# Kernel tuning notes

Measured on AMD Instinct MI355X. Metric: run time of the kernel, lower is better.

The kernel has to match this reference:

```python
import jax, jax.numpy as jnp
import numpy as np

NUM_HEADS = 16


def setup_inputs() -> dict:
    key = jax.random.key(0)
    ks = jax.random.split(key, 4)
    B, S, D = 2, 2048, 1024
    scale = 1.0 / np.sqrt(D)
    x = jax.random.normal(ks[0], (B, S, D), dtype=jnp.float32)
    Wq = jax.random.normal(ks[1], (D, D), dtype=jnp.float32) * scale
    Wk = jax.random.normal(ks[2], (D, D), dtype=jnp.float32) * scale
    Wv = jax.random.normal(ks[3], (D, D), dtype=jnp.float32) * scale
    bq = jnp.zeros((D,), dtype=jnp.float32)
    bk = jnp.zeros((D,), dtype=jnp.float32)
    bv = jnp.zeros((D,), dtype=jnp.float32)
    return {"x": x, "Wq": Wq, "bq": bq, "Wk": Wk, "bk": bk, "Wv": Wv, "bv": bv}


def _split_heads(t, H):
    B, S, D = t.shape
    return t.reshape(B, S, H, D // H).transpose(0, 2, 1, 3)  # (B,H,S,depth)


def reference(x, Wq, bq, Wk, bk, Wv, bv):
    H = NUM_HEADS
    B, S, D = x.shape
    depth = D // H
    q = _split_heads(x @ Wq + bq, H)
    k = _split_heads(x @ Wk + bk, H)
    v = _split_heads(x @ Wv + bv, H)
    # causal mask: strictly-upper-triangular ones, added as finfo.min * mask
    mask = 1.0 - jnp.tril(jnp.ones((S, S), dtype=jnp.float32))
    scores = jnp.einsum("bhqd,bhkd->bhqk", q, k) / jnp.sqrt(jnp.float32(depth))
    scores = scores + jnp.float32(np.finfo(np.float32).min) * mask
    probs = jax.nn.softmax(scores, axis=-1)
    att = jnp.einsum("bhqk,bhkd->bhqd", probs, v)
    return att.transpose(0, 2, 1, 3).reshape(B, S, D)
```

## Files before the change

### kernel.cpp

```cpp
#include <hip/hip_runtime.h>
#include <hip/hip_bf16.h>

#define B_ 2
#define S_ 2048
#define D_ 1024
#define H_ 16
#define DH 64
#define M_ (B_*S_)
#define NT_ (S_/64)

using bf16x8 = __attribute__((ext_vector_type(8))) __bf16;
using bf16x4 = __attribute__((ext_vector_type(4))) __bf16;
using f32x4  = __attribute__((ext_vector_type(4))) float;

__device__ __forceinline__ int swz(int row) { return ((row ^ (row >> 3)) & 7) << 3; }

__device__ __forceinline__ void glds16(const __bf16* g, __bf16* l) {
#if __has_builtin(__builtin_amdgcn_global_load_lds)
  __builtin_amdgcn_global_load_lds(
      (const __attribute__((address_space(1))) unsigned int*)g,
      (__attribute__((address_space(3))) unsigned int*)l, 16, 0, 0);
#else
  *(bf16x8*)l = *(const bf16x8*)g;
#endif
}

#define NBX 2048
__global__ __launch_bounds__(256) void prep(
    const float* __restrict__ x, const float* __restrict__ Wq,
    const float* __restrict__ Wk, const float* __restrict__ Wv,
    __bf16* __restrict__ xb, __bf16* __restrict__ wt) {
  int bid = blockIdx.x, tid = threadIdx.x;
  if (bid < NBX) {
    int idx = bid * 256 + tid;
    int m = idx >> 7, k = (idx & 127) * 8;
    float4 a = *(const float4*)&x[(size_t)m * D_ + k];
    float4 b = *(const float4*)&x[(size_t)m * D_ + k + 4];
    bf16x8 o;
    o[0]=(__bf16)a.x; o[1]=(__bf16)a.y; o[2]=(__bf16)a.z; o[3]=(__bf16)a.w;
    o[4]=(__bf16)b.x; o[5]=(__bf16)b.y; o[6]=(__bf16)b.z; o[7]=(__bf16)b.w;
    *(bf16x8*)&xb[(size_t)m * D_ + (k & ~63) + ((k & 63) ^ swz(m))] = o;
    return;
  }
  int wb = bid - NBX;
  int z = wb >> 8;
  int kt = (wb & 255) >> 4, nt = wb & 15;
  const float* __restrict__ W = (z == 0) ? Wq : (z == 1) ? Wk : Wv;
  __bf16* __restrict__ Wt = wt + (size_t)z * D_ * D_;
  __shared__ __bf16 Lt[64 * 66];
  int k0 = kt * 64, n0 = nt * 64;
  #pragma unroll
  for (int i = 0; i < 4; ++i) {
    int f4 = i * 256 + tid;
    int r = f4 >> 4, c4 = (f4 & 15) * 4;
    float4 v = *(const float4*)&W[(size_t)(k0 + r) * D_ + n0 + c4];
    Lt[(c4 + 0) * 66 + r] = (__bf16)v.x;
    Lt[(c4 + 1) * 66 + r] = (__bf16)v.y;
    Lt[(c4 + 2) * 66 + r] = (__bf16)v.z;
    Lt[(c4 + 3) * 66 + r] = (__bf16)v.w;
  }
  __syncthreads();
  #pragma unroll
  for (int i = 0; i < 2; ++i) {
    int idx = i * 256 + tid;
    int n = idx >> 3, kc = (idx & 7) * 8;
    int nf = n0 + n;
    bf16x8 o;
    #pragma unroll
    for (int j = 0; j < 8; ++j) o[j] = Lt[n * 66 + kc + j];
    *(bf16x8*)&Wt[(size_t)nf * D_ + k0 + (kc ^ swz(nf))] = o;
  }
}

#define BM 256
#define BN 256
#define BK 64
#define NKT (D_/BK)
#define NWG 192

__global__ __launch_bounds__(512) void qkv_gemm(
    const __bf16* __restrict__ xb, const __bf16* __restrict__ wt,
    const float* __restrict__ bq, const float* __restrict__ bk,
    const float* __restrict__ bv, __bf16* __restrict__ qk,
    __bf16* __restrict__ vt) {
  int flat = blockIdx.x;
  int sid = (flat & 7) * (NWG / 8) + (flat >> 3);
  int z = sid >> 6;
  int rem = sid & 63;
  int my = rem >> 2, nx = rem & 3;

  const __bf16* __restrict__ Wt = wt + (size_t)z * D_ * D_;
  const float* __restrict__ bias = (z == 0) ? bq : (z == 1) ? bk : bv;
  const float scale = (z == 0) ? 0.18033688f : 1.0f;

  __shared__ __bf16 SB[4][BM * BK];

  int tid = threadIdx.x, lane = tid & 63, w = tid >> 6;
  const int g = lane >> 4, ql = lane & 15;
  int m0 = my * BM, n0 = nx * BN;
  int wr = (w >> 2) * 128;
  int wc = (w & 3) * 64;

  f32x4 acc[8][4] = {};
  bf16x8 bfr[4];

#define STAGE2(buf, kt, p)                                                    \
  {                                                                           \
    int k0 = (kt) * BK;                                                       \
    _Pragma("unroll")                                                         \
    for (int q = 0; q < 2; ++q) {                                             \
      int c = 2 * (p) + q;                                                    \
      int e = ((c & 3) * 512 + tid) * 8;                                      \
      int row = e >> 6, col = e & 63;                                         \
      if (c < 4) glds16(&xb[(size_t)(m0 + row) * D_ + k0 + col], &SB[buf][e]);\
      else glds16(&Wt[(size_t)(n0 + row) * D_ + k0 + col], &SB[2 + (buf)][e]);\
    }                                                                         \
  }

#define DSB(buf, kk)                                                          \
  {                                                                           \
    _Pragma("unroll")                                                         \
    for (int ni = 0; ni < 4; ++ni) {                                          \
      int col = wc + ni * 16 + ql;                                            \
      bfr[ni] = *(const bf16x8*)&SB[2 + (buf)][col * 64 +                     \
                (((kk) * 32 + g * 8) ^ swz(col))];                            \
    }                                                                         \
  }

#define DSA4(buf, kk, mh, af)                                                 \
  {                                                                           \
    _Pragma("unroll")                                                         \
    for (int mi = 0; mi < 4; ++mi) {                                          \
      int row = wr + ((mh) * 4 + mi) * 16 + ql;                               \
      af[mi] = *(const bf16x8*)&SB[buf][row * 64 +                            \
               (((kk) * 32 + g * 8) ^ swz(row))];                             \
    }                                                                         \
  }

#define MFMA16(af, mh)                                                        \
  {                                                                           \
    __builtin_amdgcn_s_setprio(1);                                            \
    _Pragma("unroll")                                                         \
    for (int mi = 0; mi < 4; ++mi)                                            \
      _Pragma("unroll")                                                       \
      for (int ni = 0; ni < 4; ++ni)                                          \
        acc[(mh) * 4 + mi][ni] = __builtin_amdgcn_mfma_f32_16x16x32_bf16(     \
            af[mi], bfr[ni], acc[(mh) * 4 + mi][ni], 0, 0, 0);                \
    __builtin_amdgcn_s_setprio(0);                                            \
  }

  #pragma unroll
  for (int p = 0; p < 4; ++p) STAGE2(0, 0, p);

  for (int t = 0; t < NKT; ++t) {
    int cb = t & 1, nb = cb ^ 1;
    bool pf = (t + 1 < NKT);
    bf16x8 af[4];
    if (pf) STAGE2(nb, t + 1, 0);
    __builtin_amdgcn_sched_barrier(0);
    if (pf) { asm volatile("s_waitcnt vmcnt(2)" ::: "memory"); }
    else    { asm volatile("s_waitcnt vmcnt(0)" ::: "memory"); }
    __builtin_amdgcn_sched_barrier(0);
    __builtin_amdgcn_s_barrier();
    __builtin_amdgcn_sched_barrier(0);
    DSB(cb, 0);
    DSA4(cb, 0, 0, af);
    MFMA16(af, 0);
    if (pf) STAGE2(nb, t + 1, 1);
    DSA4(cb, 0, 1, af);
    __builtin_amdgcn_s_barrier();
    MFMA16(af, 1);
    if (pf) STAGE2(nb, t + 1, 2);
    DSB(cb, 1);
    DSA4(cb, 1, 0, af);
    __builtin_amdgcn_s_barrier();
    MFMA16(af, 0);
    if (pf) STAGE2(nb, t + 1, 3);
    DSA4(cb, 1, 1, af);
    __builtin_amdgcn_s_barrier();
    MFMA16(af, 1);
  }
  __syncthreads();
#undef STAGE2
#undef DSB
#undef DSA4
#undef MFMA16

  __bf16* Lt = &SB[0][0];
  const int b = m0 >> 11;
  const int sbase = m0 & 2047;
  if (z == 2) {
    #pragma unroll
    for (int mi = 0; mi < 8; ++mi) {
      #pragma unroll
      for (int ni = 0; ni < 4; ++ni) {
        int nl = wc + ni * 16 + ql;
        int ml = wr + mi * 16 + g * 4;
        float bv_ = bias[n0 + nl];
        bf16x4 p4;
        #pragma unroll
        for (int r = 0; r < 4; ++r) p4[r] = (__bf16)(acc[mi][ni][r] + bv_);
        *(bf16x4*)&Lt[nl * 256 + (ml ^ ((nl & 7) << 3))] = p4;
      }
    }
    __syncthreads();
    #pragma unroll
    for (int i = 0; i < 16; ++i) {
      int gi = i * 512 + tid;
      int n = gi >> 5, mg = (gi & 31) * 8;
      bf16x8 v = *(const bf16x8*)&Lt[n * 256 + (mg ^ ((n & 7) << 3))];
      int col = n0 + n, hh = col >> 6, dh = col & 63;
      *(bf16x8*)&vt[((size_t)(b * H_ + hh) * DH + dh) * S_ + sbase + mg] = v;
    }
  } else {
    __bf16* __restrict__ out = qk + (size_t)z * M_ * D_;
    #pragma unroll
    for (int mi = 0; mi < 8; ++mi) {
      #pragma unroll
      for (int ni = 0; ni < 4; ++ni) {
        int nl = wc + ni * 16 + ql;
        float bv_ = bias[n0 + nl];
        #pragma unroll
        for (int r = 0; r < 4; ++r) {
          int ml = wr + mi * 16 + g * 4 + r;
          Lt[ml * 256 + (nl ^ ((ml & 7) << 3))] =
              (__bf16)((acc[mi][ni][r] + bv_) * scale);
        }
      }
    }
    __syncthreads();
    #pragma unroll
    for (int i = 0; i < 16; ++i) {
      int gi = i * 512 + tid;
      int ml = gi >> 5, rest = gi & 31;
      int hh = rest >> 3, cg = (rest & 7) * 8;
      int n = hh * 64 + cg;
      bf16x8 v = *(const bf16x8*)&Lt[ml * 256 + (n ^ ((ml & 7) << 3))];
      int col = n0 + n, ho = col >> 6, dh = col & 63;
      *(bf16x8*)&out[((size_t)(b * H_ + ho) * S_ + sbase + ml) * DH + dh] = v;
    }
  }
}

__device__ __forceinline__ void attn_tile_sw(
    const bf16x8* aq, f32x4* accO, float& m_reg, float& l_reg,
    const __bf16* __restrict__ Kl, const __bf16* __restrict__ Vt,
    __bf16* __restrict__ Plw, int lane, int kv0, int qbase, bool diag) {
  const int g = lane >> 4;
  const int ql = lane & 15;
  f32x4 sfT[4];
  __builtin_amdgcn_s_setprio(1);
  #pragma unroll
  for (int f = 0; f < 4; ++f) {
    f32x4 zz = {};
    int row = f * 16 + ql;
    int sr = swz(row);
    #pragma unroll
    for (int kk = 0; kk < 2; ++kk) {
      bf16x8 ka = *(const bf16x8*)&Kl[row * 64 + ((kk * 32 + g * 8) ^ sr)];
      zz = __builtin_amdgcn_mfma_f32_16x16x32_bf16(ka, aq[kk], zz, 0, 0, 0);
    }
    sfT[f] = zz;
  }
  __builtin_amdgcn_s_setprio(0);

  if (diag) {
    int qg = qbase + ql;
    #pragma unroll
    for (int f = 0; f < 4; ++f)
      #pragma unroll
      for (int r = 0; r < 4; ++r)
        if (kv0 + f * 16 + g * 4 + r > qg) sfT[f][r] = -1e30f;
  }

  float mx = sfT[0][0];
  #pragma unroll
  for (int f = 0; f < 4; ++f)
    #pragma unroll
    for (int r = 0; r < 4; ++r) mx = fmaxf(mx, sfT[f][r]);
  mx = fmaxf(mx, __shfl_xor(mx, 16, 64));
  mx = fmaxf(mx, __shfl_xor(mx, 32, 64));
  float mnew = fmaxf(m_reg, mx);
  float alpha = exp2f(m_reg - mnew);
  m_reg = mnew;
  float rs = 0.f;
  #pragma unroll
  for (int f = 0; f < 4; ++f)
    #pragma unroll
    for (int r = 0; r < 4; ++r) {
      float p = exp2f(sfT[f][r] - mnew);
      sfT[f][r] = p;
      rs += p;
    }
  rs += __shfl_xor(rs, 16, 64);
  rs += __shfl_xor(rs, 32, 64);
  l_reg = l_reg * alpha + rs;

  const int key = (ql & 7) << 3;
  #pragma unroll
  for (int f = 0; f < 4; ++f)
    #pragma unroll
    for (int r = 0; r < 4; ++r)
      Plw[ql * 64 + ((f * 16 + g * 4 + r) ^ key)] = (__bf16)sfT[f][r];

  float ab[4];
  #pragma unroll
  for (int r = 0; r < 4; ++r) ab[r] = __shfl(alpha, g * 4 + r, 16);
  #pragma unroll
  for (int f = 0; f < 4; ++f)
    #pragma unroll
    for (int r = 0; r < 4; ++r) accO[f][r] *= ab[r];

  __builtin_amdgcn_s_setprio(1);
  #pragma unroll
  for (int kk = 0; kk < 2; ++kk) {
    bf16x8 pa = *(const bf16x8*)&Plw[ql * 64 + ((kk * 32 + g * 8) ^ key)];
    #pragma unroll
    for (int f = 0; f < 4; ++f) {
      int vrow = f * 16 + ql;
      bf16x8 vb = *(const bf16x8*)&Vt[vrow * 64 + ((kk * 32 + g * 8) ^ swz(vrow))];
      accO[f] = __builtin_amdgcn_mfma_f32_16x16x32_bf16(pa, vb, accO[f], 0, 0, 0);
    }
  }
  __builtin_amdgcn_s_setprio(0);
}

__device__ __forceinline__ void attn_out_sw(
    const f32x4* accO, float l_reg, float* __restrict__ out,
    int b, int h, int qbase, int lane) {
  float lr[4];
  #pragma unroll
  for (int r = 0; r < 4; ++r) lr[r] = __shfl(l_reg, (lane >> 4) * 4 + r, 16);
  #pragma unroll
  for (int f = 0; f < 4; ++f) {
    int dh = f * 16 + (lane & 15);
    #pragma unroll
    for (int r = 0; r < 4; ++r) {
      int qg = qbase + (lane >> 4) * 4 + r;
      out[((size_t)(b * S_ + qg)) * D_ + h * DH + dh] = accO[f][r] / lr[r];
    }
  }
}

__global__ __launch_bounds__(256) void attn(
    const __bf16* __restrict__ Q, const __bf16* __restrict__ K,
    const __bf16* __restrict__ VT, float* __restrict__ out) {
  __shared__ __bf16 Kl[64 * 64];
  __shared__ __bf16 Vt[64 * 64];
  __shared__ __bf16 Pl[4][16 * 64];

  int tid = threadIdx.x, lane = tid & 63, w = tid >> 6;
  int bx = blockIdx.x, h = blockIdx.y, b = blockIdx.z;
  int qA0 = bx * 64, qB0 = (NT_ - 1 - bx) * 64;
  size_t base = ((size_t)(b * H_ + h)) * S_ * DH;
  const __bf16* __restrict__ Qg = Q + base;
  const __bf16* __restrict__ Kg = K + base;
  const __bf16* __restrict__ VTg = VT + base;

  const int g = lane >> 4, ql = lane & 15;

  bf16x8 aqA[2], aqB[2];
  int qra = qA0 + w * 16 + ql, qrb = qB0 + w * 16 + ql;
  #pragma unroll
  for (int kk = 0; kk < 2; ++kk) {
    aqA[kk] = *(const bf16x8*)&Qg[(size_t)qra * DH + kk * 32 + g * 8];
    aqB[kk] = *(const bf16x8*)&Qg[(size_t)qrb * DH + kk * 32 + g * 8];
  }

  f32x4 accA[4] = {}, accB[4] = {};
  float mA = -1e30f, lA = 0.f, mB = -1e30f, lB = 0.f;

  const int ktA = bx, ktB = NT_ - 1 - bx;

  bf16x8 kreg[2], vreg[2];
  #pragma unroll
  for (int i = 0; i < 2; ++i) {
    int e = (i * 256 + tid) * 8;
    kreg[i] = *(const bf16x8*)&Kg[(size_t)(e >> 6) * DH + (e & 63)];
    vreg[i] = *(const bf16x8*)&VTg[(size_t)(e >> 6) * S_ + (e & 63)];
  }

  for (int kt = 0; kt <= ktB; ++kt) {
    int kv0 = kt * 64;
    #pragma unroll
    for (int i = 0; i < 2; ++i) {
      int e = (i * 256 + tid) * 8;
      int rrow = e >> 6, cc = e & 63;
      *(bf16x8*)&Kl[rrow * 64 + (cc ^ swz(rrow))] = kreg[i];
      *(bf16x8*)&Vt[rrow * 64 + (cc ^ swz(rrow))] = vreg[i];
    }
    __syncthreads();

    if (kt < ktB) {
      int kvn = kv0 + 64;
      #pragma unroll
      for (int i = 0; i < 2; ++i) {
        int e = (i * 256 + tid) * 8;
        kreg[i] = *(const bf16x8*)&Kg[(size_t)(kvn + (e >> 6)) * DH + (e & 63)];
        vreg[i] = *(const bf16x8*)&VTg[(size_t)(e >> 6) * S_ + kvn + (e & 63)];
      }
    }

    attn_tile_sw(aqB, accB, mB, lB, Kl, Vt, Pl[w], lane, kv0, qB0 + w * 16,
                 kt == ktB);
    if (kt <= ktA)
      attn_tile_sw(aqA, accA, mA, lA, Kl, Vt, Pl[w], lane, kv0, qA0 + w * 16,
                   kt == ktA);
    __syncthreads();
  }

  attn_out_sw(accA, lA, out, b, h, qA0 + w * 16, lane);
  attn_out_sw(accB, lB, out, b, h, qB0 + w * 16, lane);
}

extern "C" void kernel_launch(void* const* d_in, const int* in_sizes, int n_in,
                              void* d_out, int out_size, void* d_ws, size_t ws_size,
                              hipStream_t stream) {
  const float* x  = (const float*)d_in[0];
  const float* Wq = (const float*)d_in[1];
  const float* bq = (const float*)d_in[2];
  const float* Wk = (const float*)d_in[3];
  const float* bk = (const float*)d_in[4];
  const float* Wv = (const float*)d_in[5];
  const float* bv = (const float*)d_in[6];
  float* out = (float*)d_out;

  __bf16* xb  = (__bf16*)d_ws;
  __bf16* wt  = xb + (size_t)M_ * D_;
  __bf16* qkv = wt + (size_t)3 * D_ * D_;
  __bf16* wsq = qkv;
  __bf16* wsk = qkv + (size_t)M_ * D_;
  __bf16* vtg = qkv + (size_t)2 * M_ * D_;

  prep<<<NBX + 768, 256, 0, stream>>>(x, Wq, Wk, Wv, xb, wt);
  qkv_gemm<<<NWG, 512, 0, stream>>>(xb, wt, bq, bk, bv, qkv, vtg);
  attn<<<dim3(NT_ / 2, H_, B_), 256, 0, stream>>>(wsq, wsk, vtg, out);
}
```

Measured before the change: 180.5 us.

## Assign one query tile per attention block instead of paired tiles

The attention kernel previously paired a short and a long causal query tile per block so every block did the same amount of work. Now each block handles a single query tile, launched longest-first in reverse order, which doubles the grid and halves the register state per block (one Q fragment and one accumulator set). The Q prescale changes from log2(e)/8 to 1/8, and exp2f becomes __expf. The aim is more blocks in flight and lower register pressure, at the cost of uneven per-block work and K/V tiles being loaded twice as often in total.

```diff
diff --git a/kernel.cpp b/kernel.cpp
--- a/kernel.cpp
+++ b/kernel.cpp
@@ -91,7 +91,7 @@
 
   const __bf16* __restrict__ Wt = wt + (size_t)z * D_ * D_;
   const float* __restrict__ bias = (z == 0) ? bq : (z == 1) ? bk : bv;
-  const float scale = (z == 0) ? 0.18033688f : 1.0f;
+  const float scale = (z == 0) ? 0.125f : 1.0f;
 
   __shared__ __bf16 SB[4][BM * BK];
 
@@ -242,106 +242,6 @@
   }
 }
 
-__device__ __forceinline__ void attn_tile_sw(
-    const bf16x8* aq, f32x4* accO, float& m_reg, float& l_reg,
-    const __bf16* __restrict__ Kl, const __bf16* __restrict__ Vt,
-    __bf16* __restrict__ Plw, int lane, int kv0, int qbase, bool diag) {
-  const int g = lane >> 4;
-  const int ql = lane & 15;
-  f32x4 sfT[4];
-  __builtin_amdgcn_s_setprio(1);
-  #pragma unroll
-  for (int f = 0; f < 4; ++f) {
-    f32x4 zz = {};
-    int row = f * 16 + ql;
-    int sr = swz(row);
-    #pragma unroll
-    for (int kk = 0; kk < 2; ++kk) {
-      bf16x8 ka = *(const bf16x8*)&Kl[row * 64 + ((kk * 32 + g * 8) ^ sr)];
-      zz = __builtin_amdgcn_mfma_f32_16x16x32_bf16(ka, aq[kk], zz, 0, 0, 0);
-    }
-    sfT[f] = zz;
-  }
-  __builtin_amdgcn_s_setprio(0);
-
-  if (diag) {
-    int qg = qbase + ql;
-    #pragma unroll
-    for (int f = 0; f < 4; ++f)
-      #pragma unroll
-      for (int r = 0; r < 4; ++r)
-        if (kv0 + f * 16 + g * 4 + r > qg) sfT[f][r] = -1e30f;
-  }
-
-  float mx = sfT[0][0];
-  #pragma unroll
-  for (int f = 0; f < 4; ++f)
-    #pragma unroll
-    for (int r = 0; r < 4; ++r) mx = fmaxf(mx, sfT[f][r]);
-  mx = fmaxf(mx, __shfl_xor(mx, 16, 64));
-  mx = fmaxf(mx, __shfl_xor(mx, 32, 64));
-  float mnew = fmaxf(m_reg, mx);
-  float alpha = exp2f(m_reg - mnew);
-  m_reg = mnew;
-  float rs = 0.f;
-  #pragma unroll
-  for (int f = 0; f < 4; ++f)
-    #pragma unroll
-    for (int r = 0; r < 4; ++r) {
-      float p = exp2f(sfT[f][r] - mnew);
-      sfT[f][r] = p;
-      rs += p;
-    }
-  rs += __shfl_xor(rs, 16, 64);
-  rs += __shfl_xor(rs, 32, 64);
-  l_reg = l_reg * alpha + rs;
-
-  const int key = (ql & 7) << 3;
-  #pragma unroll
-  for (int f = 0; f < 4; ++f)
-    #pragma unroll
-    for (int r = 0; r < 4; ++r)
-      Plw[ql * 64 + ((f * 16 + g * 4 + r) ^ key)] = (__bf16)sfT[f][r];
-
-  float ab[4];
-  #pragma unroll
-  for (int r = 0; r < 4; ++r) ab[r] = __shfl(alpha, g * 4 + r, 16);
-  #pragma unroll
-  for (int f = 0; f < 4; ++f)
-    #pragma unroll
-    for (int r = 0; r < 4; ++r) accO[f][r] *= ab[r];
-
-  __builtin_amdgcn_s_setprio(1);
-  #pragma unroll
-  for (int kk = 0; kk < 2; ++kk) {
-    bf16x8 pa = *(const bf16x8*)&Plw[ql * 64 + ((kk * 32 + g * 8) ^ key)];
-    #pragma unroll
-    for (int f = 0; f < 4; ++f) {
-      int vrow = f * 16 + ql;
-      bf16x8 vb = *(const bf16x8*)&Vt[vrow * 64 + ((kk * 32 + g * 8) ^ swz(vrow))];
-      accO[f] = __builtin_amdgcn_mfma_f32_16x16x32_bf16(pa, vb, accO[f], 0, 0, 0);
-    }
-  }
-  __builtin_amdgcn_s_setprio(0);
-}
-
-__device__ __forceinline__ void attn_out_sw(
-    const f32x4* accO, float l_reg, float* __restrict__ out,
-    int b, int h, int qbase, int lane) {
-  float lr[4];
-  #pragma unroll
-  for (int r = 0; r < 4; ++r) lr[r] = __shfl(l_reg, (lane >> 4) * 4 + r, 16);
-  #pragma unroll
-  for (int f = 0; f < 4; ++f) {
-    int dh = f * 16 + (lane & 15);
-    #pragma unroll
-    for (int r = 0; r < 4; ++r) {
-      int qg = qbase + (lane >> 4) * 4 + r;
-      out[((size_t)(b * S_ + qg)) * D_ + h * DH + dh] = accO[f][r] / lr[r];
-    }
-  }
-}
-
 __global__ __launch_bounds__(256) void attn(
     const __bf16* __restrict__ Q, const __bf16* __restrict__ K,
     const __bf16* __restrict__ VT, float* __restrict__ out) {
@@ -350,27 +250,26 @@
   __shared__ __bf16 Pl[4][16 * 64];
 
   int tid = threadIdx.x, lane = tid & 63, w = tid >> 6;
-  int bx = blockIdx.x, h = blockIdx.y, b = blockIdx.z;
-  int qA0 = bx * 64, qB0 = (NT_ - 1 - bx) * 64;
+  int qt = NT_ - 1 - blockIdx.x;
+  int h = blockIdx.y, b = blockIdx.z;
+  int q0 = qt * 64;
   size_t base = ((size_t)(b * H_ + h)) * S_ * DH;
   const __bf16* __restrict__ Qg = Q + base;
   const __bf16* __restrict__ Kg = K + base;
   const __bf16* __restrict__ VTg = VT + base;
 
   const int g = lane >> 4, ql = lane & 15;
-
-  bf16x8 aqA[2], aqB[2];
-  int qra = qA0 + w * 16 + ql, qrb = qB0 + w * 16 + ql;
-  #pragma unroll
-  for (int kk = 0; kk < 2; ++kk) {
-    aqA[kk] = *(const bf16x8*)&Qg[(size_t)qra * DH + kk * 32 + g * 8];
-    aqB[kk] = *(const bf16x8*)&Qg[(size_t)qrb * DH + kk * 32 + g * 8];
-  }
-
-  f32x4 accA[4] = {}, accB[4] = {};
-  float mA = -1e30f, lA = 0.f, mB = -1e30f, lB = 0.f;
-
-  const int ktA = bx, ktB = NT_ - 1 - bx;
+  const int qbase = q0 + w * 16;
+
+  bf16x8 aq[2];
+  #pragma unroll
+  for (int kk = 0; kk < 2; ++kk)
+    aq[kk] = *(const bf16x8*)&Qg[(size_t)(qbase + ql) * DH + kk * 32 + g * 8];
+
+  f32x4 accO[4] = {};
+  float m_reg = -1e30f, l_reg = 0.f;
+
+  const int ktmax = qt;
 
   bf16x8 kreg[2], vreg[2];
   #pragma unroll
@@ -380,7 +279,7 @@
     vreg[i] = *(const bf16x8*)&VTg[(size_t)(e >> 6) * S_ + (e & 63)];
   }
 
-  for (int kt = 0; kt <= ktB; ++kt) {
+  for (int kt = 0; kt <= ktmax; ++kt) {
     int kv0 = kt * 64;
     #pragma unroll
     for (int i = 0; i < 2; ++i) {
@@ -391,7 +290,7 @@
     }
     __syncthreads();
 
-    if (kt < ktB) {
+    if (kt < ktmax) {
       int kvn = kv0 + 64;
       #pragma unroll
       for (int i = 0; i < 2; ++i) {
@@ -401,16 +300,96 @@
       }
     }
 
-    attn_tile_sw(aqB, accB, mB, lB, Kl, Vt, Pl[w], lane, kv0, qB0 + w * 16,
-                 kt == ktB);
-    if (kt <= ktA)
-      attn_tile_sw(aqA, accA, mA, lA, Kl, Vt, Pl[w], lane, kv0, qA0 + w * 16,
-                   kt == ktA);
+    f32x4 sfT[4];
+    __builtin_amdgcn_s_setprio(1);
+    #pragma unroll
+    for (int f = 0; f < 4; ++f) {
+      f32x4 zz = {};
+      int row = f * 16 + ql;
+      int sr = swz(row);
+      #pragma unroll
+      for (int kk = 0; kk < 2; ++kk) {
+        bf16x8 ka = *(const bf16x8*)&Kl[row * 64 + ((kk * 32 + g * 8) ^ sr)];
+        zz = __builtin_amdgcn_mfma_f32_16x16x32_bf16(ka, aq[kk], zz, 0, 0, 0);
+      }
+      sfT[f] = zz;
+    }
+    __builtin_amdgcn_s_setprio(0);
+
+    if (kt == ktmax) {
+      int qg = qbase + ql;
+      #pragma unroll
+      for (int f = 0; f < 4; ++f)
+        #pragma unroll
+        for (int r = 0; r < 4; ++r)
+          if (kv0 + f * 16 + g * 4 + r > qg) sfT[f][r] = -1e30f;
+    }
+
+    float mx = sfT[0][0];
+    #pragma unroll
+    for (int f = 0; f < 4; ++f)
+      #pragma unroll
+      for (int r = 0; r < 4; ++r) mx = fmaxf(mx, sfT[f][r]);
+    mx = fmaxf(mx, __shfl_xor(mx, 16, 64));
+    mx = fmaxf(mx, __shfl_xor(mx, 32, 64));
+    float mnew = fmaxf(m_reg, mx);
+    float alpha = __expf(m_reg - mnew);
+    m_reg = mnew;
+    float rs = 0.f;
+    #pragma unroll
+    for (int f = 0; f < 4; ++f)
+      #pragma unroll
+      for (int r = 0; r < 4; ++r) {
+        float p = __expf(sfT[f][r] - mnew);
+        sfT[f][r] = p;
+        rs += p;
+      }
+    rs += __shfl_xor(rs, 16, 64);
+    rs += __shfl_xor(rs, 32, 64);
+    l_reg = l_reg * alpha + rs;
+
+    const int key = (ql & 7) << 3;
+    #pragma unroll
+    for (int f = 0; f < 4; ++f)
+      #pragma unroll
+      for (int r = 0; r < 4; ++r)
+        Pl[w][ql * 64 + ((f * 16 + g * 4 + r) ^ key)] = (__bf16)sfT[f][r];
+
+    float ab[4];
+    #pragma unroll
+    for (int r = 0; r < 4; ++r) ab[r] = __shfl(alpha, g * 4 + r, 16);
+    #pragma unroll
+    for (int f = 0; f < 4; ++f)
+      #pragma unroll
+      for (int r = 0; r < 4; ++r) accO[f][r] *= ab[r];
+
+    __builtin_amdgcn_s_setprio(1);
+    #pragma unroll
+    for (int kk = 0; kk < 2; ++kk) {
+      bf16x8 pa = *(const bf16x8*)&Pl[w][ql * 64 + ((kk * 32 + g * 8) ^ key)];
+      #pragma unroll
+      for (int f = 0; f < 4; ++f) {
+        int vrow = f * 16 + ql;
+        bf16x8 vb = *(const bf16x8*)&Vt[vrow * 64 + ((kk * 32 + g * 8) ^ swz(vrow))];
+        accO[f] = __builtin_amdgcn_mfma_f32_16x16x32_bf16(pa, vb, accO[f], 0, 0, 0);
+      }
+    }
+    __builtin_amdgcn_s_setprio(0);
     __syncthreads();
   }
 
-  attn_out_sw(accA, lA, out, b, h, qA0 + w * 16, lane);
-  attn_out_sw(accB, lB, out, b, h, qB0 + w * 16, lane);
+  float lr[4];
+  #pragma unroll
+  for (int r = 0; r < 4; ++r) lr[r] = __shfl(l_reg, g * 4 + r, 16);
+  #pragma unroll
+  for (int f = 0; f < 4; ++f) {
+    int dh = f * 16 + ql;
+    #pragma unroll
+    for (int r = 0; r < 4; ++r) {
+      int qg = qbase + g * 4 + r;
+      out[((size_t)(b * S_ + qg)) * D_ + h * DH + dh] = accO[f][r] / lr[r];
+    }
+  }
 }
 
 extern "C" void kernel_launch(void* const* d_in, const int* in_sizes, int n_in,
@@ -434,5 +413,5 @@
 
   prep<<<NBX + 768, 256, 0, stream>>>(x, Wq, Wk, Wv, xb, wt);
   qkv_gemm<<<NWG, 512, 0, stream>>>(xb, wt, bq, bk, bv, qkv, vtg);
-  attn<<<dim3(NT_ / 2, H_, B_), 256, 0, stream>>>(wsq, wsk, vtg, out);
+  attn<<<dim3(NT_, H_, B_), 256, 0, stream>>>(wsq, wsk, vtg, out);
 }
```

New measurement: 213.7 us. 1.18x slower.
